# Kernel optimization log

Measured on AMD Instinct MI355X. Metric: run time of the kernel, lower is better.

The kernel has to match this reference:

```python
import jax, jax.numpy as jnp
import numpy as np
from jax import lax

N_LAYERS = 4
D_MODEL = 256
D_INNER = 512   # expand * d_model
D_STATE = 16
D_CONV = 4
DT_RANK = 16    # ceil(d_model/16)
N_FEATURES = 32
N_CLASSES = 3
BATCH, SEQ = 8, 2048


def _layernorm(x, w, b, eps=1e-5):
    mu = x.mean(-1, keepdims=True)
    var = ((x - mu) ** 2).mean(-1, keepdims=True)
    return (x - mu) * lax.rsqrt(var + eps) * w + b


def _silu(x):
    return x * jax.nn.sigmoid(x)


def _ssm(xc, xpW, dtW, dtB, A_log, D):
    # xc: (B,S,d_inner)
    xd = xc @ xpW                                    # (B,S,dt_rank+2*d_state)
    dt_r = xd[..., :DT_RANK]
    Bm = xd[..., DT_RANK:DT_RANK + D_STATE]          # (B,S,N)
    Cm = xd[..., DT_RANK + D_STATE:]                 # (B,S,N)
    dt = jax.nn.softplus(dt_r @ dtW + dtB)           # (B,S,d_inner)
    A = -jnp.exp(A_log)                              # (d_inner,N)
    dA = jnp.exp(dt[..., None] * A)                  # (B,S,d_inner,N)
    dBx = dt[..., None] * Bm[:, :, None, :] * xc[..., None]  # (B,S,d_inner,N)

    def step(h, inp):
        dA_t, dBx_t, C_t = inp                       # (B,d_inner,N),(B,d_inner,N),(B,N)
        h = dA_t * h + dBx_t
        y_t = (h * C_t[:, None, :]).sum(-1)          # (B,d_inner)
        return h, y_t

    h0 = jnp.zeros((xc.shape[0], D_INNER, D_STATE), xc.dtype)
    xs = (dA.transpose(1, 0, 2, 3), dBx.transpose(1, 0, 2, 3), Cm.transpose(1, 0, 2))
    _, ys = lax.scan(step, h0, xs)                   # (S,B,d_inner)
    y = ys.transpose(1, 0, 2)
    return y + xc * D


def _mamba_block(x, inW, convW, convB, xpW, dtW, dtB, A_log, D, outW):
    xz = x @ inW                                     # (B,S,2*d_inner)
    xs, z = xz[..., :D_INNER], xz[..., D_INNER:]
    # causal depthwise conv1d (left-pad d_conv-1)
    xp = jnp.pad(xs, ((0, 0), (D_CONV - 1, 0), (0, 0)))
    xc = lax.conv_general_dilated(
        xp, convW, window_strides=(1,), padding='VALID',
        dimension_numbers=('NWC', 'WIO', 'NWC'),
        feature_group_count=D_INNER) + convB
    xc = _silu(xc)
    y = _ssm(xc, xpW, dtW, dtB, A_log, D)
    y = y * _silu(z)
    return y @ outW


def setup_inputs() -> dict:
    key = jax.random.key(0)
    ks = jax.random.split(key, 20)
    s = 0.02
    L = N_LAYERS
    inp = {
        'x': jax.random.normal(ks[0], (BATCH, SEQ, N_FEATURES), jnp.float32),
        'in_w': jax.random.normal(ks[1], (N_FEATURES, D_MODEL), jnp.float32) * s,
        'in_b': jnp.zeros((D_MODEL,), jnp.float32),
        'ln_w': jnp.ones((L, D_MODEL), jnp.float32),
        'ln_b': jnp.zeros((L, D_MODEL), jnp.float32),
        'inW': jax.random.normal(ks[2], (L, D_MODEL, 2 * D_INNER), jnp.float32) * s,
        'convW': jax.random.normal(ks[3], (L, D_CONV, 1, D_INNER), jnp.float32) * s,
        'convB': jnp.zeros((L, D_INNER), jnp.float32),
        'xpW': jax.random.normal(ks[4], (L, D_INNER, DT_RANK + 2 * D_STATE), jnp.float32) * s,
        'dtW': jax.random.uniform(ks[5], (L, DT_RANK, D_INNER), jnp.float32,
                                  -DT_RANK ** -0.5, DT_RANK ** -0.5),
        'A_log': jnp.broadcast_to(jnp.log(jnp.arange(1, D_STATE + 1, dtype=jnp.float32)),
                                  (L, D_INNER, D_STATE)).copy(),
        'D': jnp.ones((L, D_INNER), jnp.float32),
        'outW': jax.random.normal(ks[6], (L, D_INNER, D_MODEL), jnp.float32) * s,
        'fln_w': jnp.ones((D_MODEL,), jnp.float32),
        'fln_b': jnp.zeros((D_MODEL,), jnp.float32),
        'h1W': jax.random.normal(ks[7], (D_MODEL, D_MODEL // 2), jnp.float32) * s,
        'h1b': jnp.zeros((D_MODEL // 2,), jnp.float32),
        'h2W': jax.random.normal(ks[8], (D_MODEL // 2, N_CLASSES), jnp.float32) * s,
        'h2b': jnp.zeros((N_CLASSES,), jnp.float32),
    }
    # dt bias init: inv softplus of dt ~ LogUniform(dt_min, dt_max)
    dt_min, dt_max = 1e-3, 0.1
    u = jax.random.uniform(ks[9], (L, D_INNER), jnp.float32)
    dt = jnp.clip(jnp.exp(u * (np.log(dt_max) - np.log(dt_min)) + np.log(dt_min)), 1e-4)
    inp['dtB'] = dt + jnp.log(-jnp.expm1(-dt))
    return inp


def reference(x, in_w, in_b, ln_w, ln_b, inW, convW, convB, xpW, dtW, dtB,
              A_log, D, outW, fln_w, fln_b, h1W, h1b, h2W, h2b):
    h = x @ in_w + in_b                              # (B,S,d_model); dropout is eval-mode identity
    for i in range(N_LAYERS):
        h = h + _mamba_block(_layernorm(h, ln_w[i], ln_b[i]),
                             inW[i], convW[i], convB[i], xpW[i],
                             dtW[i], dtB[i], A_log[i], D[i], outW[i])
    h = _layernorm(h, fln_w, fln_b)
    last = h[:, -1]                                  # (B,d_model)
    hidden = jax.nn.gelu(last @ h1W + h1b)
    return hidden @ h2W + h2b                        # (B,n_classes)
```

## Files before the change

### kernel.cpp

```cpp
#include <hip/hip_runtime.h>
#include <math.h>

namespace {

constexpr int NL = 4;
constexpr int DM = 256;
constexpr int DI = 512;
constexpr int DS = 16;
constexpr int DR = 16;
constexpr int NF = 32;
constexpr int NB = 8;
constexpr int T  = 2048;
constexpr int ROWS = NB * T;
constexpr int XD = DR + 2 * DS;
constexpr int NC = 64;
constexpr int CL = T / NC;
constexpr int SCN = NB * DI * DS;

constexpr float LOG2E = 1.44269504088896341f;
constexpr float LN2   = 0.69314718055994531f;

typedef __attribute__((ext_vector_type(4))) float f32x4;
typedef __attribute__((ext_vector_type(8))) short bf16x8;
typedef __attribute__((ext_vector_type(4))) short s16x4;

__device__ __forceinline__ float fexp2(float x) { return __builtin_amdgcn_exp2f(x); }
__device__ __forceinline__ float frcp(float x)  { return __builtin_amdgcn_rcpf(x); }
__device__ __forceinline__ float flog2(float x) { return __builtin_amdgcn_logf(x); }

__device__ __forceinline__ float siluf(float x) {
    return x * frcp(1.f + fexp2(-LOG2E * x));
}
__device__ __forceinline__ float softplusf(float x) {
    return fmaxf(x, 0.f) + LN2 * flog2(1.f + fexp2(-LOG2E * fabsf(x)));
}
__device__ __forceinline__ short f2bf(float f) {
    union { float f; unsigned u; } c; c.f = f;
    unsigned r = (c.u + 0x7FFFu + ((c.u >> 16) & 1u)) >> 16;
    return (short)r;
}
__device__ __forceinline__ float bf2f(short s) {
    union { unsigned u; float f; } c; c.u = ((unsigned)(unsigned short)s) << 16;
    return c.f;
}
__device__ __forceinline__ void powers16(float g, float* a) {
    float g2 = g * g, g4 = g2 * g2, g8 = g4 * g4;
    a[0] = g;        a[1] = g2;       a[2] = g * g2;   a[3] = g4;
    a[4] = g * g4;   a[5] = g2 * g4;  a[6] = a[2] * g4; a[7] = g8;
    a[8] = g * g8;   a[9] = g2 * g8;  a[10] = a[2] * g8; a[11] = g4 * g8;
    a[12] = a[4] * g8; a[13] = a[5] * g8; a[14] = a[6] * g8; a[15] = g8 * g8;
}

constexpr int PN1 = NL * 1024 * DM;
constexpr int PN2 = NL * 64 * DI;
constexpr int PN3 = NL * DM * DI;
constexpr int PN4 = DM * NF;
constexpr int PN5 = NL * DI * DR;
constexpr int PN6 = NL * DI * DS;
constexpr int PN7 = ROWS * NF;
constexpr int PTOT = PN1 + PN2 + PN3 + PN4 + PN5 + PN6 + PN7;

__global__ void prep_all(const float* __restrict__ inW, const float* __restrict__ xpW,
                         const float* __restrict__ outW, const float* __restrict__ in_w,
                         const float* __restrict__ dtW, const float* __restrict__ A_log,
                         const float* __restrict__ x,
                         short* __restrict__ inWt, short* __restrict__ xpWt,
                         short* __restrict__ outWt, short* __restrict__ inwT,
                         float* __restrict__ dtWt, float* __restrict__ negA2,
                         short* __restrict__ xb)
{
    int idx = blockIdx.x * 256 + threadIdx.x;
    if (idx < PN1) {
        int l = idx / (1024 * DM), r = idx - l * (1024 * DM);
        int n = r / DM, k = r - n * DM;
        inWt[idx] = f2bf(inW[(size_t)l * DM * 1024 + (size_t)k * 1024 + n]);
        return;
    }
    idx -= PN1;
    if (idx < PN2) {
        int l = idx / (64 * DI), r = idx - l * (64 * DI);
        int n = r / DI, k = r - n * DI;
        xpWt[idx] = (n < XD) ? f2bf(xpW[(size_t)l * DI * XD + (size_t)k * XD + n]) : (short)0;
        return;
    }
    idx -= PN2;
    if (idx < PN3) {
        int l = idx / (DM * DI), r = idx - l * (DM * DI);
        int n = r / DI, k = r - n * DI;
        outWt[idx] = f2bf(outW[(size_t)l * DI * DM + (size_t)k * DM + n]);
        return;
    }
    idx -= PN3;
    if (idx < PN4) {
        int n = idx / NF, k = idx - n * NF;
        inwT[idx] = f2bf(in_w[(size_t)k * DM + n]);
        return;
    }
    idx -= PN4;
    if (idx < PN5) {
        int l = idx / (DI * DR), r0 = idx - l * (DI * DR);
        int d = r0 / DR, rr = r0 - d * DR;
        dtWt[idx] = dtW[(size_t)l * DR * DI + (size_t)rr * DI + d];
        return;
    }
    idx -= PN5;
    if (idx < PN6) {
        negA2[idx] = -LOG2E * fexp2(LOG2E * A_log[idx]);
        return;
    }
    idx -= PN6;
    if (idx < PN7) xb[idx] = f2bf(x[idx]);
}

template <int EP, int BM, int BN>
__global__ void gemm_mfma(const short* __restrict__ A, const short* __restrict__ Bt,
                          float* __restrict__ C, short* __restrict__ Cs0,
                          short* __restrict__ Cs1, const float* __restrict__ bias,
                          int K, int lda, int ldc, int Ncut, int NXB, int NYB)
{
    constexpr int MF  = BM / 32;
    constexpr int NFr = BN / 32;
    __shared__ short smem[BM * 40 + BN * 40];
    const int bid = blockIdx.x;
    const int xcd = bid & 7, j = bid >> 3;
    const int by = xcd * (NYB >> 3) + j / NXB;
    const int bx = j - (j / NXB) * NXB;
    const int m0 = by * BM;
    const int n0 = bx * BN;

    const int tid = threadIdx.x;
    const int lane = tid & 63, w = tid >> 6;
    const int wr = w >> 1, wc = w & 1;
    const int lr = lane & 15, lk = lane >> 4;

    f32x4 acc[MF][NFr] = {};
    for (int k0 = 0; k0 < K; k0 += 32) {
        __syncthreads();
#pragma unroll
        for (int i = 0; i < BM / 64; ++i) {
            int c = tid + i * 256;
            int row = c >> 2, seg = c & 3;
            bf16x8 v = *(const bf16x8*)(A + (size_t)(m0 + row) * lda + k0 + seg * 8);
            *(bf16x8*)(&smem[row * 40 + seg * 8]) = v;
        }
#pragma unroll
        for (int i = 0; i < BN / 64; ++i) {
            int c = tid + i * 256;
            int row = c >> 2, seg = c & 3;
            bf16x8 v = *(const bf16x8*)(Bt + (size_t)(n0 + row) * K + k0 + seg * 8);
            *(bf16x8*)(&smem[BM * 40 + row * 40 + seg * 8]) = v;
        }
        __syncthreads();
        bf16x8 af[MF], bfr[NFr];
#pragma unroll
        for (int m = 0; m < MF; ++m)
            af[m] = *(const bf16x8*)(&smem[(wr * (BM / 2) + m * 16 + lr) * 40 + lk * 8]);
#pragma unroll
        for (int n = 0; n < NFr; ++n)
            bfr[n] = *(const bf16x8*)(&smem[BM * 40 + (wc * (BN / 2) + n * 16 + lr) * 40 + lk * 8]);
#pragma unroll
        for (int m = 0; m < MF; ++m)
#pragma unroll
            for (int n = 0; n < NFr; ++n)
                acc[m][n] = __builtin_amdgcn_mfma_f32_16x16x32_bf16(af[m], bfr[n], acc[m][n], 0, 0, 0);
    }
#pragma unroll
    for (int m = 0; m < MF; ++m) {
#pragma unroll
        for (int n = 0; n < NFr; ++n) {
            const int col = n0 + wc * (BN / 2) + n * 16 + lr;
#pragma unroll
            for (int j2 = 0; j2 < 4; ++j2) {
                const int row = m0 + wr * (BM / 2) + m * 16 + lk * 4 + j2;
                const float v = acc[m][n][j2];
                if (EP == 0) {
                    if (col < DI) Cs0[(size_t)row * DI + col] = f2bf(v);
                    else          Cs1[(size_t)row * DI + col - DI] = f2bf(siluf(v));
                } else if (EP == 1) {
                    if (col < Ncut) C[(size_t)row * ldc + col] = v;
                } else if (EP == 2) {
                    C[(size_t)row * ldc + col] += v;
                } else {
                    C[(size_t)row * ldc + col] = v + bias[col];
                }
            }
        }
    }
}

__global__ void layernorm_kernel(const float* __restrict__ x,
                                 const float* __restrict__ w,
                                 const float* __restrict__ b,
                                 short* __restrict__ out)
{
    const int row = blockIdx.x;
    const int t = threadIdx.x;
    const int wid = t >> 6, lane = t & 63;
    __shared__ float red[4];

    float v = x[row * DM + t];
    float s = v;
#pragma unroll
    for (int o = 32; o >= 1; o >>= 1) s += __shfl_xor(s, o);
    if (lane == 0) red[wid] = s;
    __syncthreads();
    float mu = (red[0] + red[1] + red[2] + red[3]) * (1.f / DM);
    __syncthreads();

    float d = v - mu;
    float q = d * d;
#pragma unroll
    for (int o = 32; o >= 1; o >>= 1) q += __shfl_xor(q, o);
    if (lane == 0) red[wid] = q;
    __syncthreads();
    float var = (red[0] + red[1] + red[2] + red[3]) * (1.f / DM);

    out[row * DM + t] = f2bf(d * (1.f / sqrtf(var + 1e-5f)) * w[t] + b[t]);
}

__global__ void conv_silu_kernel(const short* __restrict__ xsb,
                                 const float* __restrict__ W,
                                 const float* __restrict__ Bc,
                                 short* __restrict__ xcb)
{
    const int idx = blockIdx.x * 256 + threadIdx.x;
    const int c4 = idx & (DI / 4 - 1);
    const int bt = idx >> 7;
    const int t = bt & (T - 1);
    const int c = c4 * 4;
    f32x4 acc = *(const f32x4*)(Bc + c);
#pragma unroll
    for (int k = 0; k < 4; ++k) {
        int tt = t + k - 3;
        if (tt >= 0) {
            s16x4 v = *(const s16x4*)(xsb + (size_t)(bt + k - 3) * DI + c);
            f32x4 wv = *(const f32x4*)(W + k * DI + c);
#pragma unroll
            for (int q = 0; q < 4; ++q) acc[q] += bf2f(v[q]) * wv[q];
        }
    }
    s16x4 o;
#pragma unroll
    for (int q = 0; q < 4; ++q) o[q] = f2bf(siluf(acc[q]));
    *(s16x4*)(xcb + (size_t)idx * 4) = o;
}

__global__ void scan_pass1(const float* __restrict__ xd,
                           const short* __restrict__ xcb,
                           const float* __restrict__ negA2,
                           const float* __restrict__ dtWt,
                           const float* __restrict__ dtB,
                           float* __restrict__ S, float* __restrict__ sdtb)
{
    __shared__ float lds[CL][32];
    const int d = blockIdx.x * 256 + threadIdx.x;
    const int c = blockIdx.y;
    const int b = blockIdx.z;
    const int row0 = b * T + c * CL;

    {
        int t = threadIdx.x >> 3, seg = threadIdx.x & 7;
        *(f32x4*)&lds[t][seg * 4] =
            *(const f32x4*)(xd + (size_t)(row0 + t) * XD + seg * 4);
    }
    float A2[DS], h[DS], wcol[DR];
#pragma unroll
    for (int q = 0; q < 4; ++q) {
        *(f32x4*)&A2[q * 4]   = *(const f32x4*)(negA2 + d * DS + q * 4);
        *(f32x4*)&wcol[q * 4] = *(const f32x4*)(dtWt + d * DR + q * 4);
    }
    bool fastb = true;
#pragma unroll
    for (int s = 1; s < DS; ++s)
        fastb = fastb && (fabsf(A2[s] - A2[0] * (float)(s + 1)) <= 1e-4f * fabsf(A2[s]));
    const bool fast = __all(fastb);
#pragma unroll
    for (int s = 0; s < DS; ++s) h[s] = 0.f;
    const float dtBd = dtB[d];
    float sdt = 0.f;
    __syncthreads();

    for (int t = 0; t < CL; ++t) {
        float xcv = bf2f(xcb[(size_t)(row0 + t) * DI + d]);
        float accd = dtBd;
#pragma unroll
        for (int q = 0; q < 4; ++q) {
            f32x4 xr = *(const f32x4*)&lds[t][q * 4];
            accd += xr[0] * wcol[q * 4] + xr[1] * wcol[q * 4 + 1]
                  + xr[2] * wcol[q * 4 + 2] + xr[3] * wcol[q * 4 + 3];
        }
        float dtv = softplusf(accd);
        float dx = dtv * xcv;
        sdt += dtv;
        float a[DS];
        if (fast) powers16(fexp2(dtv * A2[0]), a);
        else {
#pragma unroll
            for (int s = 0; s < DS; ++s) a[s] = fexp2(dtv * A2[s]);
        }
#pragma unroll
        for (int q = 0; q < 4; ++q) {
            f32x4 Bv = *(const f32x4*)&lds[t][16 + q * 4];
#pragma unroll
            for (int s = 0; s < 4; ++s)
                h[q * 4 + s] = a[q * 4 + s] * h[q * 4 + s] + dx * Bv[s];
        }
    }
    const size_t base = (size_t)c * SCN + ((size_t)b * DI + d) * DS;
#pragma unroll
    for (int q = 0; q < 4; ++q)
        *(f32x4*)(S + base + q * 4) = *(f32x4*)&h[q * 4];
    sdtb[c * (NB * DI) + b * DI + d] = sdt;
}

__global__ void scan_combine(float* __restrict__ S, const float* __restrict__ sdtb,
                             const float* __restrict__ negA2)
{
    const int idx3 = blockIdx.x * blockDim.x + threadIdx.x;
    const int bd = idx3 >> 4;
    const float A2c = negA2[(bd & (DI - 1)) * DS + (idx3 & 15)];
    float h = 0.f;
    for (int c = 0; c < NC; ++c) {
        float sc = S[(size_t)c * SCN + idx3];
        float pc = fexp2(A2c * sdtb[c * (NB * DI) + bd]);
        S[(size_t)c * SCN + idx3] = h;
        h = pc * h + sc;
    }
}

__global__ void scan_pass2(const float* __restrict__ xd,
                           const short* __restrict__ xcb,
                           const float* __restrict__ negA2,
                           const float* __restrict__ dtWt,
                           const float* __restrict__ dtB,
                           const float* __restrict__ Dv,
                           const float* __restrict__ H,
                           const short* __restrict__ zgb,
                           short* __restrict__ yb)
{
    __shared__ float lds[CL][48];
    const int d = blockIdx.x * 256 + threadIdx.x;
    const int c = blockIdx.y;
    const int b = blockIdx.z;
    const int row0 = b * T + c * CL;

    for (int c0 = threadIdx.x; c0 < CL * 12; c0 += 256) {
        int t = c0 / 12, seg = c0 - t * 12;
        *(f32x4*)&lds[t][seg * 4] =
            *(const f32x4*)(xd + (size_t)(row0 + t) * XD + seg * 4);
    }
    float A2[DS], h[DS], wcol[DR];
#pragma unroll
    for (int q = 0; q < 4; ++q) {
        *(f32x4*)&A2[q * 4]   = *(const f32x4*)(negA2 + d * DS + q * 4);
        *(f32x4*)&wcol[q * 4] = *(const f32x4*)(dtWt + d * DR + q * 4);
    }
    bool fastb = true;
#pragma unroll
    for (int s = 1; s < DS; ++s)
        fastb = fastb && (fabsf(A2[s] - A2[0] * (float)(s + 1)) <= 1e-4f * fabsf(A2[s]));
    const bool fast = __all(fastb);
    const size_t base = (size_t)c * SCN + ((size_t)b * DI + d) * DS;
#pragma unroll
    for (int q = 0; q < 4; ++q)
        *(f32x4*)&h[q * 4] = *(const f32x4*)(H + base + q * 4);
    const float dtBd = dtB[d];
    const float Dd = Dv[d];
    __syncthreads();

    for (int t = 0; t < CL; ++t) {
        const size_t row = (size_t)(row0 + t);
        float xcv = bf2f(xcb[row * DI + d]);
        float zg  = bf2f(zgb[row * DI + d]);
        float accd = dtBd;
#pragma unroll
        for (int q = 0; q < 4; ++q) {
            f32x4 xr = *(const f32x4*)&lds[t][q * 4];
            accd += xr[0] * wcol[q * 4] + xr[1] * wcol[q * 4 + 1]
                  + xr[2] * wcol[q * 4 + 2] + xr[3] * wcol[q * 4 + 3];
        }
        float dtv = softplusf(accd);
        float dx = dtv * xcv;
        float a[DS];
        if (fast) powers16(fexp2(dtv * A2[0]), a);
        else {
#pragma unroll
            for (int s = 0; s < DS; ++s) a[s] = fexp2(dtv * A2[s]);
        }
        float acc0 = 0.f, acc1 = 0.f, acc2 = 0.f, acc3 = 0.f;
#pragma unroll
        for (int q = 0; q < 4; ++q) {
            f32x4 Bv = *(const f32x4*)&lds[t][16 + q * 4];
            f32x4 Cv = *(const f32x4*)&lds[t][32 + q * 4];
            h[q * 4 + 0] = a[q * 4 + 0] * h[q * 4 + 0] + dx * Bv[0];
            acc0 += h[q * 4 + 0] * Cv[0];
            h[q * 4 + 1] = a[q * 4 + 1] * h[q * 4 + 1] + dx * Bv[1];
            acc1 += h[q * 4 + 1] * Cv[1];
            h[q * 4 + 2] = a[q * 4 + 2] * h[q * 4 + 2] + dx * Bv[2];
            acc2 += h[q * 4 + 2] * Cv[2];
            h[q * 4 + 3] = a[q * 4 + 3] * h[q * 4 + 3] + dx * Bv[3];
            acc3 += h[q * 4 + 3] * Cv[3];
        }
        float yv = (acc0 + acc1) + (acc2 + acc3);
        yb[row * DI + d] = f2bf((yv + xcv * Dd) * zg);
    }
}

__global__ void head_kernel(const float* __restrict__ h,
                            const float* __restrict__ fw, const float* __restrict__ fb,
                            const float* __restrict__ h1W, const float* __restrict__ h1b,
                            const float* __restrict__ h2W, const float* __restrict__ h2b,
                            float* __restrict__ out)
{
    const int bi = blockIdx.x;
    const int t = threadIdx.x;
    const int wid = t >> 6, lane = t & 63;
    __shared__ float red[4];
    __shared__ float ln[DM];
    __shared__ float hid[DM / 2];

    const float* row = h + ((bi + 1) * T - 1) * DM;
    float v = row[t];
    float s = v;
#pragma unroll
    for (int o = 32; o >= 1; o >>= 1) s += __shfl_xor(s, o);
    if (lane == 0) red[wid] = s;
    __syncthreads();
    float mu = (red[0] + red[1] + red[2] + red[3]) * (1.f / DM);
    __syncthreads();
    float d = v - mu;
    float q = d * d;
#pragma unroll
    for (int o = 32; o >= 1; o >>= 1) q += __shfl_xor(q, o);
    if (lane == 0) red[wid] = q;
    __syncthreads();
    float var = (red[0] + red[1] + red[2] + red[3]) * (1.f / DM);
    ln[t] = d * (1.f / sqrtf(var + 1e-5f)) * fw[t] + fb[t];
    __syncthreads();

    if (t < DM / 2) {
        float acc = h1b[t];
        for (int k = 0; k < DM; ++k) acc += ln[k] * h1W[k * (DM / 2) + t];
        float x3 = acc * acc * acc;
        hid[t] = 0.5f * acc * (1.f + tanhf(0.7978845608028654f * (acc + 0.044715f * x3)));
    }
    __syncthreads();
    if (t < 3) {
        float acc = h2b[t];
        for (int k = 0; k < DM / 2; ++k) acc += hid[k] * h2W[k * 3 + t];
        out[bi * 3 + t] = acc;
    }
}

}

extern "C" void kernel_launch(void* const* d_in, const int* in_sizes, int n_in,
                              void* d_out, int out_size, void* d_ws, size_t ws_size,
                              hipStream_t stream)
{
    (void)in_sizes; (void)n_in; (void)out_size; (void)ws_size;
    const float* x     = (const float*)d_in[0];
    const float* in_w  = (const float*)d_in[1];
    const float* in_b  = (const float*)d_in[2];
    const float* ln_w  = (const float*)d_in[3];
    const float* ln_b  = (const float*)d_in[4];
    const float* inW   = (const float*)d_in[5];
    const float* convW = (const float*)d_in[6];
    const float* convB = (const float*)d_in[7];
    const float* xpW   = (const float*)d_in[8];
    const float* dtW   = (const float*)d_in[9];
    const float* A_log = (const float*)d_in[10];
    const float* Dv    = (const float*)d_in[11];
    const float* outW  = (const float*)d_in[12];
    const float* fln_w = (const float*)d_in[13];
    const float* fln_b = (const float*)d_in[14];
    const float* h1W   = (const float*)d_in[15];
    const float* h1b   = (const float*)d_in[16];
    const float* h2W   = (const float*)d_in[17];
    const float* h2b   = (const float*)d_in[18];
    const float* dtB   = (const float*)d_in[19];
    float* out = (float*)d_out;

    float* w = (float*)d_ws;
    float* hbuf  = w;  w += ROWS * DM;
    float* xd    = w;  w += ROWS * XD;
    float* S     = w;  w += (size_t)SCN * NC;
    float* sdtb  = w;  w += NC * NB * DI;
    float* negA2 = w;  w += NL * DI * DS;
    float* dtWt  = w;  w += NL * DI * DR;
    short* xlnb  = (short*)w;
    short* xb    = xlnb + (size_t)ROWS * DM;
    short* xsb   = xb   + (size_t)ROWS * NF;
    short* zgb   = xsb  + (size_t)ROWS * DI;
    short* xcb   = zgb  + (size_t)ROWS * DI;
    short* yb    = xcb  + (size_t)ROWS * DI;
    short* inWt  = yb   + (size_t)ROWS * DI;
    short* xpWt  = inWt + (size_t)NL * 1024 * DM;
    short* outWt = xpWt + (size_t)NL * 64 * DI;
    short* inwT  = outWt + (size_t)NL * DM * DI;

    prep_all<<<(PTOT + 255) / 256, 256, 0, stream>>>(
        inW, xpW, outW, in_w, dtW, A_log, x,
        inWt, xpWt, outWt, inwT, dtWt, negA2, xb);

    gemm_mfma<3, 128, 64><<<(DM / 64) * (ROWS / 128), 256, 0, stream>>>(
        xb, inwT, hbuf, nullptr, nullptr, in_b, NF, NF, DM, 0, DM / 64, ROWS / 128);

    for (int i = 0; i < NL; ++i) {
        layernorm_kernel<<<ROWS, DM, 0, stream>>>(hbuf, ln_w + i * DM, ln_b + i * DM, xlnb);

        gemm_mfma<0, 128, 128><<<(1024 / 128) * (ROWS / 128), 256, 0, stream>>>(
            xlnb, inWt + (size_t)i * 1024 * DM, nullptr, xsb, zgb, nullptr,
            DM, DM, 0, 0, 1024 / 128, ROWS / 128);

        conv_silu_kernel<<<ROWS * DI / 1024, 256, 0, stream>>>(
            xsb, convW + i * 4 * DI, convB + i * DI, xcb);

        gemm_mfma<1, 64, 64><<<1 * (ROWS / 64), 256, 0, stream>>>(
            xcb, xpWt + (size_t)i * 64 * DI, xd, nullptr, nullptr, nullptr,
            DI, DI, XD, XD, 1, ROWS / 64);

        scan_pass1<<<dim3(DI / 256, NC, NB), 256, 0, stream>>>(
            xd, xcb, negA2 + i * DI * DS, dtWt + i * DI * DR, dtB + i * DI, S, sdtb);
        scan_combine<<<SCN / 256, 256, 0, stream>>>(S, sdtb, negA2 + i * DI * DS);
        scan_pass2<<<dim3(DI / 256, NC, NB), 256, 0, stream>>>(
            xd, xcb, negA2 + i * DI * DS, dtWt + i * DI * DR, dtB + i * DI,
            Dv + i * DI, S, zgb, yb);

        gemm_mfma<2, 128, 128><<<(DM / 128) * (ROWS / 128), 256, 0, stream>>>(
            yb, outWt + (size_t)i * DM * DI, hbuf, nullptr, nullptr, nullptr,
            DI, DI, DM, 0, DM / 128, ROWS / 128);
    }

    head_kernel<<<NB, DM, 0, stream>>>(hbuf, fln_w, fln_b, h1W, h1b, h2W, h2b, out);
}
```

Measured before the change: 620.5 us.

## Fold LayerNorm into in-proj GEMM using row stats from residual epilogue

Removes the per-layer LayerNorm kernel. The residual-producing GEMM epilogues now write a bf16 copy of h and atomically accumulate per-row sum and sum of squares. The in-proj GEMM then applies normalization algebraically, using ln_w folded into the weights plus precomputed column sums and a bias term. This saves one full read and write of the activations per layer, at the cost of atomics, a less numerically stable variance formula (E[x²]−mu²), and applying LN after bf16 rounding of the raw h rather than the normalized value.

```diff
diff --git a/kernel.cpp b/kernel.cpp
--- a/kernel.cpp
+++ b/kernel.cpp
@@ -58,22 +58,26 @@
 constexpr int PN5 = NL * DI * DR;
 constexpr int PN6 = NL * DI * DS;
 constexpr int PN7 = ROWS * NF;
-constexpr int PTOT = PN1 + PN2 + PN3 + PN4 + PN5 + PN6 + PN7;
+constexpr int PN8 = NL * 1024 * 2;
+constexpr int PN9 = ROWS * 2;
+constexpr int PTOT = PN1 + PN2 + PN3 + PN4 + PN5 + PN6 + PN7 + PN8 + PN9;
 
 __global__ void prep_all(const float* __restrict__ inW, const float* __restrict__ xpW,
                          const float* __restrict__ outW, const float* __restrict__ in_w,
                          const float* __restrict__ dtW, const float* __restrict__ A_log,
-                         const float* __restrict__ x,
+                         const float* __restrict__ x, const float* __restrict__ ln_w,
+                         const float* __restrict__ ln_b,
                          short* __restrict__ inWt, short* __restrict__ xpWt,
                          short* __restrict__ outWt, short* __restrict__ inwT,
                          float* __restrict__ dtWt, float* __restrict__ negA2,
-                         short* __restrict__ xb)
+                         short* __restrict__ xb, float* __restrict__ colsum,
+                         float* __restrict__ bb, float* __restrict__ stats)
 {
     int idx = blockIdx.x * 256 + threadIdx.x;
     if (idx < PN1) {
         int l = idx / (1024 * DM), r = idx - l * (1024 * DM);
         int n = r / DM, k = r - n * DM;
-        inWt[idx] = f2bf(inW[(size_t)l * DM * 1024 + (size_t)k * 1024 + n]);
+        inWt[idx] = f2bf(ln_w[l * DM + k] * inW[(size_t)l * DM * 1024 + (size_t)k * 1024 + n]);
         return;
     }
     idx -= PN1;
@@ -109,13 +113,28 @@
         return;
     }
     idx -= PN6;
-    if (idx < PN7) xb[idx] = f2bf(x[idx]);
+    if (idx < PN7) { xb[idx] = f2bf(x[idx]); return; }
+    idx -= PN7;
+    if (idx < PN8) {
+        int l = idx / 2048, r = idx - l * 2048;
+        int which = r >> 10, n = r & 1023;
+        const float* wv = which ? (ln_b + l * DM) : (ln_w + l * DM);
+        float s = 0.f;
+        for (int k = 0; k < DM; ++k)
+            s += wv[k] * inW[(size_t)l * DM * 1024 + (size_t)k * 1024 + n];
+        (which ? bb : colsum)[l * 1024 + n] = s;
+        return;
+    }
+    idx -= PN8;
+    if (idx < PN9) stats[idx] = 0.f;
 }
 
 template <int EP, int BM, int BN>
 __global__ void gemm_mfma(const short* __restrict__ A, const short* __restrict__ Bt,
                           float* __restrict__ C, short* __restrict__ Cs0,
                           short* __restrict__ Cs1, const float* __restrict__ bias,
+                          float* __restrict__ stats, const float* __restrict__ colsum,
+                          const float* __restrict__ bb, short* __restrict__ hbw,
                           int K, int lda, int ldc, int Ncut, int NXB, int NYB)
 {
     constexpr int MF  = BM / 32;
@@ -167,55 +186,46 @@
 #pragma unroll
     for (int m = 0; m < MF; ++m) {
 #pragma unroll
-        for (int n = 0; n < NFr; ++n) {
-            const int col = n0 + wc * (BN / 2) + n * 16 + lr;
-#pragma unroll
-            for (int j2 = 0; j2 < 4; ++j2) {
-                const int row = m0 + wr * (BM / 2) + m * 16 + lk * 4 + j2;
-                const float v = acc[m][n][j2];
+        for (int j2 = 0; j2 < 4; ++j2) {
+            const int row = m0 + wr * (BM / 2) + m * 16 + lk * 4 + j2;
+            float mu = 0.f, rsv = 0.f;
+            if (EP == 0) {
+                float s1 = stats[row * 2], s2 = stats[row * 2 + 1];
+                mu = s1 * (1.f / DM);
+                float var = s2 * (1.f / DM) - mu * mu;
+                rsv = 1.f / sqrtf(var + 1e-5f);
+            }
+            float s1 = 0.f, s2 = 0.f;
+#pragma unroll
+            for (int n = 0; n < NFr; ++n) {
+                const int col = n0 + wc * (BN / 2) + n * 16 + lr;
+                float v = acc[m][n][j2];
                 if (EP == 0) {
+                    v = rsv * v - rsv * mu * colsum[col] + bb[col];
                     if (col < DI) Cs0[(size_t)row * DI + col] = f2bf(v);
                     else          Cs1[(size_t)row * DI + col - DI] = f2bf(siluf(v));
                 } else if (EP == 1) {
                     if (col < Ncut) C[(size_t)row * ldc + col] = v;
-                } else if (EP == 2) {
-                    C[(size_t)row * ldc + col] += v;
                 } else {
-                    C[(size_t)row * ldc + col] = v + bias[col];
+                    if (EP == 2) v += C[(size_t)row * ldc + col];
+                    else         v += bias[col];
+                    C[(size_t)row * ldc + col] = v;
+                    hbw[(size_t)row * ldc + col] = f2bf(v);
+                    s1 += v; s2 += v * v;
                 }
             }
-        }
-    }
-}
-
-__global__ void layernorm_kernel(const float* __restrict__ x,
-                                 const float* __restrict__ w,
-                                 const float* __restrict__ b,
-                                 short* __restrict__ out)
-{
-    const int row = blockIdx.x;
-    const int t = threadIdx.x;
-    const int wid = t >> 6, lane = t & 63;
-    __shared__ float red[4];
-
-    float v = x[row * DM + t];
-    float s = v;
-#pragma unroll
-    for (int o = 32; o >= 1; o >>= 1) s += __shfl_xor(s, o);
-    if (lane == 0) red[wid] = s;
-    __syncthreads();
-    float mu = (red[0] + red[1] + red[2] + red[3]) * (1.f / DM);
-    __syncthreads();
-
-    float d = v - mu;
-    float q = d * d;
-#pragma unroll
-    for (int o = 32; o >= 1; o >>= 1) q += __shfl_xor(q, o);
-    if (lane == 0) red[wid] = q;
-    __syncthreads();
-    float var = (red[0] + red[1] + red[2] + red[3]) * (1.f / DM);
-
-    out[row * DM + t] = f2bf(d * (1.f / sqrtf(var + 1e-5f)) * w[t] + b[t]);
+            if (EP == 2 || EP == 3) {
+                s1 += __shfl_xor(s1, 1); s2 += __shfl_xor(s2, 1);
+                s1 += __shfl_xor(s1, 2); s2 += __shfl_xor(s2, 2);
+                s1 += __shfl_xor(s1, 4); s2 += __shfl_xor(s2, 4);
+                s1 += __shfl_xor(s1, 8); s2 += __shfl_xor(s2, 8);
+                if (lr == 0) {
+                    atomicAdd(&stats[row * 2], s1);
+                    atomicAdd(&stats[row * 2 + 1], s2);
+                }
+            }
+        }
+    }
 }
 
 __global__ void conv_silu_kernel(const short* __restrict__ xsb,
@@ -336,13 +346,17 @@
                            const float* __restrict__ Dv,
                            const float* __restrict__ H,
                            const short* __restrict__ zgb,
-                           short* __restrict__ yb)
+                           short* __restrict__ yb,
+                           float* __restrict__ stats)
 {
     __shared__ float lds[CL][48];
     const int d = blockIdx.x * 256 + threadIdx.x;
     const int c = blockIdx.y;
     const int b = blockIdx.z;
     const int row0 = b * T + c * CL;
+
+    if (blockIdx.x == 0 && threadIdx.x < CL * 2)
+        stats[(size_t)(row0 + (threadIdx.x >> 1)) * 2 + (threadIdx.x & 1)] = 0.f;
 
     for (int c0 = threadIdx.x; c0 < CL * 12; c0 += 256) {
         int t = c0 / 12, seg = c0 - t * 12;
@@ -482,14 +496,17 @@
     float* out = (float*)d_out;
 
     float* w = (float*)d_ws;
-    float* hbuf  = w;  w += ROWS * DM;
-    float* xd    = w;  w += ROWS * XD;
-    float* S     = w;  w += (size_t)SCN * NC;
-    float* sdtb  = w;  w += NC * NB * DI;
-    float* negA2 = w;  w += NL * DI * DS;
-    float* dtWt  = w;  w += NL * DI * DR;
-    short* xlnb  = (short*)w;
-    short* xb    = xlnb + (size_t)ROWS * DM;
+    float* hbuf   = w;  w += ROWS * DM;
+    float* xd     = w;  w += ROWS * XD;
+    float* S      = w;  w += (size_t)SCN * NC;
+    float* sdtb   = w;  w += NC * NB * DI;
+    float* negA2  = w;  w += NL * DI * DS;
+    float* dtWt   = w;  w += NL * DI * DR;
+    float* colsum = w;  w += NL * 1024;
+    float* bbv    = w;  w += NL * 1024;
+    float* stats  = w;  w += ROWS * 2;
+    short* hb    = (short*)w;
+    short* xb    = hb   + (size_t)ROWS * DM;
     short* xsb   = xb   + (size_t)ROWS * NF;
     short* zgb   = xsb  + (size_t)ROWS * DI;
     short* xcb   = zgb  + (size_t)ROWS * DI;
@@ -500,17 +517,17 @@
     short* inwT  = outWt + (size_t)NL * DM * DI;
 
     prep_all<<<(PTOT + 255) / 256, 256, 0, stream>>>(
-        inW, xpW, outW, in_w, dtW, A_log, x,
-        inWt, xpWt, outWt, inwT, dtWt, negA2, xb);
+        inW, xpW, outW, in_w, dtW, A_log, x, ln_w, ln_b,
+        inWt, xpWt, outWt, inwT, dtWt, negA2, xb, colsum, bbv, stats);
 
     gemm_mfma<3, 128, 64><<<(DM / 64) * (ROWS / 128), 256, 0, stream>>>(
-        xb, inwT, hbuf, nullptr, nullptr, in_b, NF, NF, DM, 0, DM / 64, ROWS / 128);
+        xb, inwT, hbuf, nullptr, nullptr, in_b, stats, nullptr, nullptr, hb,
+        NF, NF, DM, 0, DM / 64, ROWS / 128);
 
     for (int i = 0; i < NL; ++i) {
-        layernorm_kernel<<<ROWS, DM, 0, stream>>>(hbuf, ln_w + i * DM, ln_b + i * DM, xlnb);
-
         gemm_mfma<0, 128, 128><<<(1024 / 128) * (ROWS / 128), 256, 0, stream>>>(
-            xlnb, inWt + (size_t)i * 1024 * DM, nullptr, xsb, zgb, nullptr,
+            hb, inWt + (size_t)i * 1024 * DM, nullptr, xsb, zgb, nullptr,
+            stats, colsum + i * 1024, bbv + i * 1024, nullptr,
             DM, DM, 0, 0, 1024 / 128, ROWS / 128);
 
         conv_silu_kernel<<<ROWS * DI / 1024, 256, 0, stream>>>(
@@ -518,18 +535,18 @@
 
         gemm_mfma<1, 64, 64><<<1 * (ROWS / 64), 256, 0, stream>>>(
             xcb, xpWt + (size_t)i * 64 * DI, xd, nullptr, nullptr, nullptr,
-            DI, DI, XD, XD, 1, ROWS / 64);
+            nullptr, nullptr, nullptr, nullptr, DI, DI, XD, XD, 1, ROWS / 64);
 
         scan_pass1<<<dim3(DI / 256, NC, NB), 256, 0, stream>>>(
             xd, xcb, negA2 + i * DI * DS, dtWt + i * DI * DR, dtB + i * DI, S, sdtb);
         scan_combine<<<SCN / 256, 256, 0, stream>>>(S, sdtb, negA2 + i * DI * DS);
         scan_pass2<<<dim3(DI / 256, NC, NB), 256, 0, stream>>>(
             xd, xcb, negA2 + i * DI * DS, dtWt + i * DI * DR, dtB + i * DI,
-            Dv + i * DI, S, zgb, yb);
+            Dv + i * DI, S, zgb, yb, stats);
 
         gemm_mfma<2, 128, 128><<<(DM / 128) * (ROWS / 128), 256, 0, stream>>>(
             yb, outWt + (size_t)i * DM * DI, hbuf, nullptr, nullptr, nullptr,
-            DI, DI, DM, 0, DM / 128, ROWS / 128);
+            stats, nullptr, nullptr, hb, DI, DI, DM, 0, DM / 128, ROWS / 128);
     }
 
     head_kernel<<<NB, DM, 0, stream>>>(hbuf, fln_w, fln_b, h1W, h1b, h2W, h2b, out);
```

Result: faster. 592.9 us, median of 2 (-4.4%).
